# Optimization experiments

Hardware: AMD Instinct MI355X
Metric: run time of the kernel (lower is better)

## Reference

```python
import jax, jax.numpy as jnp
import numpy as np

H = 512   # hidden_size
E = 256   # embedding_size
V = 32000 # vocab_size
L = 1024  # max_length (encoder seq len)
B = 64    # batch


def setup_inputs() -> dict:
    key = jax.random.key(0)
    ks = jax.random.split(key, 18)
    n = lambda i, shape, s=0.05: (jax.random.normal(ks[i], shape, dtype=jnp.float32) * s)
    return {
        "input": jax.random.randint(ks[0], (B, 1), 0, V),
        "last_output_context": n(1, (1, B, H), 1.0),
        "last_hidden": n(2, (1, B, H), 1.0),
        "last_cell_state": n(3, (1, B, H), 1.0),
        "encoder_outputs": n(4, (L, B, H), 1.0),
        "emb": n(5, (V, E)),
        "W_ih": n(6, (4 * H, E + H)),
        "W_hh": n(7, (4 * H, H)),
        "b_ih": n(8, (4 * H,)),
        "b_hh": n(9, (4 * H,)),
        "W_attn": n(10, (H, 2 * H)),
        "b_attn": n(11, (H,)),
        "beta": n(12, (H, 1), 1.0),
        "W_oc": n(13, (H, 2 * H)),
        "b_oc": n(14, (H,)),
        "W_out": n(15, (V, H)),
        "b_out": n(16, (V,)),
    }


def reference(input, last_output_context, last_hidden, last_cell_state,
              encoder_outputs, emb, W_ih, W_hh, b_ih, b_hh,
              W_attn, b_attn, beta, W_oc, b_oc, W_out, b_out):
    # embedding lookup: (B,1) -> (B,E)  (permute(1,0,2) then squeeze step dim)
    tok = emb[input[:, 0]]                                   # (B, E)
    x = jnp.concatenate([tok, last_output_context[0]], axis=1)  # (B, E+H)
    # single-step LSTM (PyTorch gate order i, f, g, o)
    gates = x @ W_ih.T + last_hidden[0] @ W_hh.T + b_ih + b_hh  # (B, 4H)
    i_g, f_g, g_g, o_g = jnp.split(gates, 4, axis=1)
    i_g = jax.nn.sigmoid(i_g)
    f_g = jax.nn.sigmoid(f_g)
    g_g = jnp.tanh(g_g)
    o_g = jax.nn.sigmoid(o_g)
    c = f_g * last_cell_state[0] + i_g * g_g                  # (B, H)
    h = o_g * jnp.tanh(c)                                     # (B, H) == rnn_output
    # additive attention, vectorized over the seq_len loop
    h_tiled = jnp.broadcast_to(h[None], (L, B, H))
    cat = jnp.concatenate([h_tiled, encoder_outputs], axis=-1)  # (L, B, 2H)
    energy = jnp.tanh(cat @ W_attn.T + b_attn) @ beta           # (L, B, 1)
    attn_w = jax.nn.softmax(energy[..., 0], axis=0)             # (L, B) softmax over seq
    # context = bmm(attn_weights, encoder_outputs)
    context = jnp.einsum('lb,lbh->bh', attn_w, encoder_outputs)  # (B, H)
    co = jnp.tanh(jnp.concatenate([h, context], axis=1) @ W_oc.T + b_oc)  # (B, H)
    output = jax.nn.log_softmax(co @ W_out.T + b_out, axis=1)    # (B, V)
    return output, co[None], h[None], c[None]
```

## Files before the change

kernel.cpp:

```cpp
#include <hip/hip_runtime.h>
#include <hip/hip_bf16.h>
#include <cstddef>

#define H   512
#define E   256
#define V   32000
#define L   1024
#define B   64
#define KX  768
#define M_TOT 65536

typedef __attribute__((ext_vector_type(8))) _Float16 half8v;
typedef __attribute__((ext_vector_type(4))) float f32x4;

__global__ __launch_bounds__(256) void k_conv_w(const float* __restrict__ W_attn,
                                                unsigned short* __restrict__ Wf) {
    int e0 = blockIdx.x * 2048 + threadIdx.x * 8;
    int j = e0 >> 9, k = e0 & 511;
    const float* src = &W_attn[(size_t)j * (2 * H) + H + k];
    float4 x0 = *reinterpret_cast<const float4*>(src);
    float4 x1 = *reinterpret_cast<const float4*>(src + 4);
    float xs[8] = {x0.x, x0.y, x0.z, x0.w, x1.x, x1.y, x1.z, x1.w};
    union { half8v v; _Float16 u[8]; } hv;
    #pragma unroll
    for (int i = 0; i < 8; ++i) hv.u[i] = (_Float16)xs[i];
    *reinterpret_cast<half8v*>(&Wf[e0]) = hv.v;
}

__global__ __launch_bounds__(256) void k_build(const int* __restrict__ inp,
                                               const float* __restrict__ loc,
                                               const float* __restrict__ hprev,
                                               const float* __restrict__ emb,
                                               float* __restrict__ xprevT) {
    int gid = blockIdx.x * 256 + threadIdx.x;
    int k = gid >> 6, b = gid & 63;
    float v;
    if (k < 256)      v = emb[(size_t)inp[b] * E + k];
    else if (k < 768) v = loc[b * H + (k - 256)];
    else              v = hprev[b * H + (k - 768)];
    xprevT[gid] = v;
}

__global__ __launch_bounds__(256) void k_lstm(const float* __restrict__ W_ih,
                                              const float* __restrict__ W_hh,
                                              const float* __restrict__ b_ih,
                                              const float* __restrict__ b_hh,
                                              const float* __restrict__ xprevT,
                                              const float* __restrict__ cprev,
                                              float* __restrict__ h_out,
                                              float* __restrict__ c_out,
                                              float* __restrict__ hnewT) {
    int u = blockIdx.x;
    int w = threadIdx.x >> 6;
    int b = threadIdx.x & 63;
    int j = w * 512 + u;
    float a0 = 0.f, a1 = 0.f, a2 = 0.f, a3 = 0.f;
    const float* Wr = &W_ih[(size_t)j * KX];
    for (int k = 0; k < KX; k += 4) {
        float4 wv = *reinterpret_cast<const float4*>(&Wr[k]);
        a0 += wv.x * xprevT[(k + 0) * 64 + b];
        a1 += wv.y * xprevT[(k + 1) * 64 + b];
        a2 += wv.z * xprevT[(k + 2) * 64 + b];
        a3 += wv.w * xprevT[(k + 3) * 64 + b];
    }
    const float* Wr2 = &W_hh[(size_t)j * H];
    const float* hT = &xprevT[KX * 64];
    for (int k = 0; k < H; k += 4) {
        float4 wv = *reinterpret_cast<const float4*>(&Wr2[k]);
        a0 += wv.x * hT[(k + 0) * 64 + b];
        a1 += wv.y * hT[(k + 1) * 64 + b];
        a2 += wv.z * hT[(k + 2) * 64 + b];
        a3 += wv.w * hT[(k + 3) * 64 + b];
    }
    float acc = b_ih[j] + b_hh[j] + ((a0 + a1) + (a2 + a3));
    __shared__ float gs[4][64];
    gs[w][b] = acc;
    __syncthreads();
    if (threadIdx.x < 64) {
        float ig = 1.f / (1.f + __expf(-gs[0][b]));
        float fg = 1.f / (1.f + __expf(-gs[1][b]));
        float gg = tanhf(gs[2][b]);
        float og = 1.f / (1.f + __expf(-gs[3][b]));
        float c = fg * cprev[b * H + u] + ig * gg;
        float h = og * tanhf(c);
        c_out[b * H + u] = c;
        h_out[b * H + u] = h;
        hnewT[u * 64 + b] = h;
    }
}

__global__ __launch_bounds__(256) void k_hw(const float* __restrict__ W_attn,
                                            const float* __restrict__ b_attn,
                                            const float* __restrict__ hT,
                                            float* __restrict__ hW_jb) {
    int j = blockIdx.x * 4 + (threadIdx.x >> 6);
    int b = threadIdx.x & 63;
    float a0 = 0.f, a1 = 0.f, a2 = 0.f, a3 = 0.f;
    const float* Wr = &W_attn[(size_t)j * (2 * H)];
    for (int k = 0; k < H; k += 4) {
        float4 wv = *reinterpret_cast<const float4*>(&Wr[k]);
        a0 += wv.x * hT[(k + 0) * 64 + b];
        a1 += wv.y * hT[(k + 1) * 64 + b];
        a2 += wv.z * hT[(k + 2) * 64 + b];
        a3 += wv.w * hT[(k + 3) * 64 + b];
    }
    hW_jb[j * 64 + b] = b_attn[j] + ((a0 + a1) + (a2 + a3));
}

#define BKE 32
#define PITCH 40

__global__ __launch_bounds__(256, 4) void k_energy_v4(
        const float* __restrict__ enc,
        const unsigned short* __restrict__ Wf,
        const float* __restrict__ hW,
        const float* __restrict__ beta,
        float* __restrict__ partial_e) {
    __shared__ unsigned short Ah[128 * PITCH];
    __shared__ unsigned short Bh[128 * PITCH];
    __shared__ float red[2][128];

    const int tid  = threadIdx.x;
    const int lane = tid & 63;
    const int wave = tid >> 6;
    const int wm = wave >> 1;
    const int wn = wave & 1;
    const int mt = blockIdx.x >> 2;
    const int jt = blockIdx.x & 3;
    const int m0 = mt * 128;
    const int j0 = jt * 128;

    const int srow = tid >> 2;
    const int skc  = tid & 3;

    float4 ra0[2], ra1[2];
    half8v rb[2];
    #pragma unroll
    for (int p = 0; p < 2; ++p) {
        int row = p * 64 + srow;
        const float* asrc = &enc[(size_t)(m0 + row) * H + skc * 8];
        ra0[p] = *reinterpret_cast<const float4*>(asrc);
        ra1[p] = *reinterpret_cast<const float4*>(asrc + 4);
        rb[p] = *reinterpret_cast<const half8v*>(&Wf[(size_t)(j0 + row) * H + skc * 8]);
    }

    f32x4 acc[4][4];
    #pragma unroll
    for (int i = 0; i < 4; ++i)
        #pragma unroll
        for (int j = 0; j < 4; ++j) acc[i][j] = (f32x4){0.f, 0.f, 0.f, 0.f};

    for (int k0 = 0; k0 < H; k0 += BKE) {
        __syncthreads();
        #pragma unroll
        for (int p = 0; p < 2; ++p) {
            float xs[8] = {ra0[p].x, ra0[p].y, ra0[p].z, ra0[p].w,
                           ra1[p].x, ra1[p].y, ra1[p].z, ra1[p].w};
            union { half8v v; _Float16 u[8]; } hv;
            #pragma unroll
            for (int i = 0; i < 8; ++i) hv.u[i] = (_Float16)xs[i];
            int off = (p * 64 + srow) * PITCH + skc * 8;
            *reinterpret_cast<half8v*>(&Ah[off]) = hv.v;
            *reinterpret_cast<half8v*>(&Bh[off]) = rb[p];
        }
        __syncthreads();
        if (k0 + BKE < H) {
            int kn = k0 + BKE;
            #pragma unroll
            for (int p = 0; p < 2; ++p) {
                int row = p * 64 + srow;
                const float* asrc = &enc[(size_t)(m0 + row) * H + kn + skc * 8];
                ra0[p] = *reinterpret_cast<const float4*>(asrc);
                ra1[p] = *reinterpret_cast<const float4*>(asrc + 4);
                rb[p] = *reinterpret_cast<const half8v*>(&Wf[(size_t)(j0 + row) * H + kn + skc * 8]);
            }
        }
        const int fr = lane & 15;
        const int kb = (lane >> 4) * 8;
        half8v a_h[4], b_h[4];
        #pragma unroll
        for (int mf = 0; mf < 4; ++mf) {
            int off = (wm * 64 + mf * 16 + fr) * PITCH + kb;
            a_h[mf] = *reinterpret_cast<const half8v*>(&Ah[off]);
        }
        #pragma unroll
        for (int nf = 0; nf < 4; ++nf) {
            int off = (wn * 64 + nf * 16 + fr) * PITCH + kb;
            b_h[nf] = *reinterpret_cast<const half8v*>(&Bh[off]);
        }
        #pragma unroll
        for (int mf = 0; mf < 4; ++mf)
            #pragma unroll
            for (int nf = 0; nf < 4; ++nf)
                acc[mf][nf] = __builtin_amdgcn_mfma_f32_16x16x32_f16(
                    a_h[mf], b_h[nf], acc[mf][nf], 0, 0, 0);
    }
    float psum[4][4];
    #pragma unroll
    for (int i = 0; i < 4; ++i)
        #pragma unroll
        for (int r = 0; r < 4; ++r) psum[i][r] = 0.f;
    #pragma unroll
    for (int nf = 0; nf < 4; ++nf) {
        int jj = j0 + wn * 64 + nf * 16 + (lane & 15);
        float bet = beta[jj];
        #pragma unroll
        for (int mf = 0; mf < 4; ++mf) {
            int b_base = (wm * 64 + mf * 16 + (lane >> 4) * 4) & 63;
            float4 hw4 = *reinterpret_cast<const float4*>(&hW[jj * 64 + b_base]);
            float hwv[4] = {hw4.x, hw4.y, hw4.z, hw4.w};
            #pragma unroll
            for (int r = 0; r < 4; ++r) {
                float e = acc[mf][nf][r] + hwv[r];
                float ex = __expf(2.f * e);
                psum[mf][r] += bet * (1.f - 2.f / (ex + 1.f));
            }
        }
    }
    #pragma unroll
    for (int mf = 0; mf < 4; ++mf)
        #pragma unroll
        for (int r = 0; r < 4; ++r) {
            float v = psum[mf][r];
            v += __shfl_xor(v, 1);
            v += __shfl_xor(v, 2);
            v += __shfl_xor(v, 4);
            v += __shfl_xor(v, 8);
            psum[mf][r] = v;
        }
    __syncthreads();
    if ((lane & 15) == 0) {
        #pragma unroll
        for (int mf = 0; mf < 4; ++mf)
            #pragma unroll
            for (int r = 0; r < 4; ++r)
                red[wn][wm * 64 + mf * 16 + (lane >> 4) * 4 + r] = psum[mf][r];
    }
    __syncthreads();
    if (tid < 128)
        partial_e[(size_t)jt * M_TOT + m0 + tid] = red[0][tid] + red[1][tid];
}

__global__ __launch_bounds__(256) void k_softmax_l(const float* __restrict__ partial_e,
                                                   float* __restrict__ attn_w) {
    int b = blockIdx.x;
    int tid = threadIdx.x;
    float el[4];
    float m = -1e30f;
    #pragma unroll
    for (int i = 0; i < 4; ++i) {
        int l = i * 256 + tid;
        float e = 0.f;
        #pragma unroll
        for (int nb = 0; nb < 4; ++nb)
            e += partial_e[(size_t)nb * M_TOT + l * 64 + b];
        el[i] = e;
        m = fmaxf(m, e);
    }
    #pragma unroll
    for (int s = 1; s < 64; s <<= 1) m = fmaxf(m, __shfl_xor(m, s));
    __shared__ float redm[4];
    if ((tid & 63) == 0) redm[tid >> 6] = m;
    __syncthreads();
    m = fmaxf(fmaxf(redm[0], redm[1]), fmaxf(redm[2], redm[3]));
    float s = 0.f;
    #pragma unroll
    for (int i = 0; i < 4; ++i) { el[i] = __expf(el[i] - m); s += el[i]; }
    #pragma unroll
    for (int sh = 1; sh < 64; sh <<= 1) s += __shfl_xor(s, sh);
    __shared__ float reds[4];
    if ((tid & 63) == 0) reds[tid >> 6] = s;
    __syncthreads();
    s = reds[0] + reds[1] + reds[2] + reds[3];
    float inv = 1.f / s;
    #pragma unroll
    for (int i = 0; i < 4; ++i)
        attn_w[(i * 256 + tid) * 64 + b] = el[i] * inv;
}

__global__ __launch_bounds__(128) void k_ctx_part(const float* __restrict__ attn_w,
                                                  const float* __restrict__ enc,
                                                  float* __restrict__ ctx_part) {
    int chunk = blockIdx.x, b = blockIdx.y;
    int h = threadIdx.x * 4;
    float4 acc = {0.f, 0.f, 0.f, 0.f};
    for (int i = 0; i < 32; ++i) {
        int l = chunk * 32 + i;
        float w = attn_w[l * 64 + b];
        float4 e4 = *reinterpret_cast<const float4*>(
            &enc[((size_t)l * 64 + b) * H + h]);
        acc.x += w * e4.x;
        acc.y += w * e4.y;
        acc.z += w * e4.z;
        acc.w += w * e4.w;
    }
    *reinterpret_cast<float4*>(&ctx_part[((size_t)(chunk * 64 + b)) * H + h]) = acc;
}

__global__ __launch_bounds__(256) void k_ctx_reduce(const float* __restrict__ ctx_part,
                                                    float* __restrict__ ctxT) {
    int gid = blockIdx.x * 256 + threadIdx.x;
    int b = gid >> 9, h = gid & 511;
    float s = 0.f;
    for (int c = 0; c < 32; ++c)
        s += ctx_part[((size_t)(c * 64 + b)) * H + h];
    ctxT[h * 64 + b] = s;
}

__global__ __launch_bounds__(256) void k_co(const float* __restrict__ W_oc,
                                            const float* __restrict__ b_oc,
                                            const float* __restrict__ hT,
                                            const float* __restrict__ ctxT,
                                            float* __restrict__ co_out) {
    int j = blockIdx.x * 4 + (threadIdx.x >> 6);
    int b = threadIdx.x & 63;
    float a0 = 0.f, a1 = 0.f, a2 = 0.f, a3 = 0.f;
    const float* Wr = &W_oc[(size_t)j * (2 * H)];
    for (int k = 0; k < H; k += 4) {
        float4 wv = *reinterpret_cast<const float4*>(&Wr[k]);
        a0 += wv.x * hT[(k + 0) * 64 + b];
        a1 += wv.y * hT[(k + 1) * 64 + b];
        a2 += wv.z * hT[(k + 2) * 64 + b];
        a3 += wv.w * hT[(k + 3) * 64 + b];
    }
    const float* Wr2 = Wr + H;
    for (int k = 0; k < H; k += 4) {
        float4 wv = *reinterpret_cast<const float4*>(&Wr2[k]);
        a0 += wv.x * ctxT[(k + 0) * 64 + b];
        a1 += wv.y * ctxT[(k + 1) * 64 + b];
        a2 += wv.z * ctxT[(k + 2) * 64 + b];
        a3 += wv.w * ctxT[(k + 3) * 64 + b];
    }
    co_out[b * H + j] = tanhf(b_oc[j] + ((a0 + a1) + (a2 + a3)));
}

__global__ __launch_bounds__(256) void k_logits_v2(const float* __restrict__ co,
                                                   const float* __restrict__ W_out,
                                                   const float* __restrict__ b_out,
                                                   float* __restrict__ logits) {
    __shared__ unsigned short Ah[64 * PITCH];
    __shared__ unsigned short Bh[64 * PITCH];

    const int tid  = threadIdx.x;
    const int lane = tid & 63;
    const int wave = tid >> 6;
    const int wm = wave >> 1;
    const int wn = wave & 1;
    const int j0 = blockIdx.x * 64;

    const int srow = tid >> 2;
    const int skc  = tid & 3;

    float4 ra0, ra1, rb0, rb1;
    {
        const float* as = &co[(size_t)srow * H + skc * 8];
        ra0 = *reinterpret_cast<const float4*>(as);
        ra1 = *reinterpret_cast<const float4*>(as + 4);
        const float* bs = &W_out[(size_t)(j0 + srow) * H + skc * 8];
        rb0 = *reinterpret_cast<const float4*>(bs);
        rb1 = *reinterpret_cast<const float4*>(bs + 4);
    }

    f32x4 acc[2][2];
    #pragma unroll
    for (int i = 0; i < 2; ++i)
        #pragma unroll
        for (int j = 0; j < 2; ++j) acc[i][j] = (f32x4){0.f, 0.f, 0.f, 0.f};

    for (int k0 = 0; k0 < H; k0 += BKE) {
        __syncthreads();
        {
            float xs[8] = {ra0.x, ra0.y, ra0.z, ra0.w, ra1.x, ra1.y, ra1.z, ra1.w};
            union { half8v v; _Float16 u[8]; } ha;
            #pragma unroll
            for (int i = 0; i < 8; ++i) ha.u[i] = (_Float16)xs[i];
            float ys[8] = {rb0.x, rb0.y, rb0.z, rb0.w, rb1.x, rb1.y, rb1.z, rb1.w};
            union { half8v v; _Float16 u[8]; } hb;
            #pragma unroll
            for (int i = 0; i < 8; ++i) hb.u[i] = (_Float16)ys[i];
            int off = srow * PITCH + skc * 8;
            *reinterpret_cast<half8v*>(&Ah[off]) = ha.v;
            *reinterpret_cast<half8v*>(&Bh[off]) = hb.v;
        }
        __syncthreads();
        if (k0 + BKE < H) {
            int kn = k0 + BKE;
            const float* as = &co[(size_t)srow * H + kn + skc * 8];
            ra0 = *reinterpret_cast<const float4*>(as);
            ra1 = *reinterpret_cast<const float4*>(as + 4);
            const float* bs = &W_out[(size_t)(j0 + srow) * H + kn + skc * 8];
            rb0 = *reinterpret_cast<const float4*>(bs);
            rb1 = *reinterpret_cast<const float4*>(bs + 4);
        }
        const int fr = lane & 15;
        const int kb = (lane >> 4) * 8;
        half8v a_h[2], b_h[2];
        #pragma unroll
        for (int mf = 0; mf < 2; ++mf) {
            int off = (wm * 32 + mf * 16 + fr) * PITCH + kb;
            a_h[mf] = *reinterpret_cast<const half8v*>(&Ah[off]);
        }
        #pragma unroll
        for (int nf = 0; nf < 2; ++nf) {
            int off = (wn * 32 + nf * 16 + fr) * PITCH + kb;
            b_h[nf] = *reinterpret_cast<const half8v*>(&Bh[off]);
        }
        #pragma unroll
        for (int mf = 0; mf < 2; ++mf)
            #pragma unroll
            for (int nf = 0; nf < 2; ++nf)
                acc[mf][nf] = __builtin_amdgcn_mfma_f32_16x16x32_f16(
                    a_h[mf], b_h[nf], acc[mf][nf], 0, 0, 0);
    }
    #pragma unroll
    for (int nf = 0; nf < 2; ++nf) {
        int j = j0 + wn * 32 + nf * 16 + (lane & 15);
        float bo = b_out[j];
        #pragma unroll
        for (int mf = 0; mf < 2; ++mf) {
            int mbase = wm * 32 + mf * 16 + (lane >> 4) * 4;
            #pragma unroll
            for (int r = 0; r < 4; ++r)
                logits[(size_t)(mbase + r) * V + j] = acc[mf][nf][r] + bo;
        }
    }
}

__global__ __launch_bounds__(256) void k_lsm_part(const float* __restrict__ logits,
                                                  float* __restrict__ pmax,
                                                  float* __restrict__ psum) {
    int chunk = blockIdx.x, b = blockIdx.y;
    int tid = threadIdx.x;
    const float* row = &logits[(size_t)b * V + chunk * 4000];
    float v[16];
    float m = -1e30f;
    #pragma unroll
    for (int t = 0; t < 16; ++t) {
        int i = t * 256 + tid;
        v[t] = (i < 4000) ? row[i] : -1e30f;
        m = fmaxf(m, v[t]);
    }
    #pragma unroll
    for (int s = 1; s < 64; s <<= 1) m = fmaxf(m, __shfl_xor(m, s));
    __shared__ float redm[4];
    if ((tid & 63) == 0) redm[tid >> 6] = m;
    __syncthreads();
    m = fmaxf(fmaxf(redm[0], redm[1]), fmaxf(redm[2], redm[3]));
    float s = 0.f;
    #pragma unroll
    for (int t = 0; t < 16; ++t) s += __expf(v[t] - m);
    #pragma unroll
    for (int sh = 1; sh < 64; sh <<= 1) s += __shfl_xor(s, sh);
    __shared__ float reds[4];
    if ((tid & 63) == 0) reds[tid >> 6] = s;
    __syncthreads();
    if (tid == 0) {
        pmax[chunk * 64 + b] = m;
        psum[chunk * 64 + b] = reds[0] + reds[1] + reds[2] + reds[3];
    }
}

__global__ __launch_bounds__(64) void k_lsm_final(const float* __restrict__ pmax,
                                                  const float* __restrict__ psum,
                                                  float* __restrict__ lse) {
    int b = threadIdx.x;
    float m = -1e30f;
    #pragma unroll
    for (int c = 0; c < 8; ++c) m = fmaxf(m, pmax[c * 64 + b]);
    float s = 0.f;
    #pragma unroll
    for (int c = 0; c < 8; ++c) s += psum[c * 64 + b] * __expf(pmax[c * 64 + b] - m);
    lse[b] = m + __logf(s);
}

__global__ __launch_bounds__(256) void k_lsm_write(const float* __restrict__ logits,
                                                   const float* __restrict__ lse,
                                                   float* __restrict__ out) {
    size_t i4 = ((size_t)blockIdx.x * 256 + threadIdx.x) * 4;
    int b = (int)(i4 / V);
    float l = lse[b];
    float4 x = *reinterpret_cast<const float4*>(&logits[i4]);
    x.x -= l; x.y -= l; x.z -= l; x.w -= l;
    *reinterpret_cast<float4*>(&out[i4]) = x;
}

extern "C" void kernel_launch(void* const* d_in, const int* in_sizes, int n_in,
                              void* d_out, int out_size, void* d_ws, size_t ws_size,
                              hipStream_t stream) {
    const int*   inp    = (const int*)  d_in[0];
    const float* loc    = (const float*)d_in[1];
    const float* hprev  = (const float*)d_in[2];
    const float* cprev  = (const float*)d_in[3];
    const float* enc    = (const float*)d_in[4];
    const float* emb    = (const float*)d_in[5];
    const float* W_ih   = (const float*)d_in[6];
    const float* W_hh   = (const float*)d_in[7];
    const float* b_ih   = (const float*)d_in[8];
    const float* b_hh   = (const float*)d_in[9];
    const float* W_attn = (const float*)d_in[10];
    const float* b_attn = (const float*)d_in[11];
    const float* beta   = (const float*)d_in[12];
    const float* W_oc   = (const float*)d_in[13];
    const float* b_oc   = (const float*)d_in[14];
    const float* W_out  = (const float*)d_in[15];
    const float* b_out  = (const float*)d_in[16];

    float* out = (float*)d_out;
    float* out_co = out + (size_t)B * V;
    float* out_h  = out_co + B * H;
    float* out_c  = out_h  + B * H;

    float* ws = (float*)d_ws;
    float* xprevT = ws;
    float* hnewT  = xprevT + 1280 * 64;
    float* hW     = hnewT  + H * 64;
    float* pe     = hW     + H * 64;
    float* attnw  = pe     + 4 * M_TOT;
    float* ctxp   = attnw  + M_TOT;
    float* ctxT   = ctxp   + 32 * 64 * H;
    float* logits = ctxT   + H * 64;
    float* pmax   = logits + (size_t)B * V;
    float* psum   = pmax   + 512;
    float* lse    = psum   + 512;
    unsigned short* Wf = (unsigned short*)(lse + 64);

    k_conv_w<<<128, 256, 0, stream>>>(W_attn, Wf);
    k_build <<<320, 256, 0, stream>>>(inp, loc, hprev, emb, xprevT);
    k_lstm  <<<512, 256, 0, stream>>>(W_ih, W_hh, b_ih, b_hh, xprevT, cprev,
                                      out_h, out_c, hnewT);
    k_hw    <<<128, 256, 0, stream>>>(W_attn, b_attn, hnewT, hW);
    k_energy_v4<<<2048, 256, 0, stream>>>(enc, Wf, hW, beta, pe);
    k_softmax_l<<<64, 256, 0, stream>>>(pe, attnw);
    k_ctx_part <<<dim3(32, 64), 128, 0, stream>>>(attnw, enc, ctxp);
    k_ctx_reduce<<<128, 256, 0, stream>>>(ctxp, ctxT);
    k_co    <<<128, 256, 0, stream>>>(W_oc, b_oc, hnewT, ctxT, out_co);
    k_logits_v2<<<500, 256, 0, stream>>>(out_co, W_out, b_out, logits);
    k_lsm_part<<<dim3(8, 64), 256, 0, stream>>>(logits, pmax, psum);
    k_lsm_final<<<1, 64, 0, stream>>>(pmax, psum, lse);
    k_lsm_write<<<2000, 256, 0, stream>>>(logits, lse, out);
}
```

Baseline: 257.1 us.

## Deepen energy GEMM K-tile, remap blocks per XCD, raise MFMA priority

The attention-energy GEMM kernel now uses a K step of 64 instead of 32, which halves the number of barrier/stage iterations and issues 32 MFMAs per stage. It also remaps block indices so the four j-tiles of one M tile, which read the same encoder rows, are consecutive in the per-XCD (bid&7) ordering, to improve L2 reuse of the encoder rows. s_setprio is raised around the MFMA burst. In exchange, more registers are needed for the prefetch buffers and LDS use roughly doubles, which may reduce occupancy under launch_bounds(256,4). The logits kernel keeps its old tile constants under new names.

```diff
diff --git a/kernel.cpp b/kernel.cpp
--- a/kernel.cpp
+++ b/kernel.cpp
@@ -107,17 +107,17 @@
     hW_jb[j * 64 + b] = b_attn[j] + ((a0 + a1) + (a2 + a3));
 }
 
-#define BKE 32
-#define PITCH 40
-
-__global__ __launch_bounds__(256, 4) void k_energy_v4(
+#define BKE 64
+#define PITCHE 72
+
+__global__ __launch_bounds__(256, 4) void k_energy_v5(
         const float* __restrict__ enc,
         const unsigned short* __restrict__ Wf,
         const float* __restrict__ hW,
         const float* __restrict__ beta,
         float* __restrict__ partial_e) {
-    __shared__ unsigned short Ah[128 * PITCH];
-    __shared__ unsigned short Bh[128 * PITCH];
+    __shared__ unsigned short Ah[128 * PITCHE];
+    __shared__ unsigned short Bh[128 * PITCHE];
     __shared__ float red[2][128];
 
     const int tid  = threadIdx.x;
@@ -125,23 +125,26 @@
     const int wave = tid >> 6;
     const int wm = wave >> 1;
     const int wn = wave & 1;
-    const int mt = blockIdx.x >> 2;
-    const int jt = blockIdx.x & 3;
+    const int bid = blockIdx.x;
+    const int xcd = bid & 7;
+    const int loc = bid >> 3;
+    const int mt  = xcd * 64 + (loc >> 2);
+    const int jt  = loc & 3;
     const int m0 = mt * 128;
     const int j0 = jt * 128;
 
-    const int srow = tid >> 2;
-    const int skc  = tid & 3;
-
-    float4 ra0[2], ra1[2];
-    half8v rb[2];
-    #pragma unroll
-    for (int p = 0; p < 2; ++p) {
-        int row = p * 64 + srow;
-        const float* asrc = &enc[(size_t)(m0 + row) * H + skc * 8];
+    const int q  = tid & 7;
+    const int r0 = tid >> 3;
+
+    float4 ra0[4], ra1[4];
+    half8v rb[4];
+    #pragma unroll
+    for (int p = 0; p < 4; ++p) {
+        int row = p * 32 + r0;
+        const float* asrc = &enc[(size_t)(m0 + row) * H + q * 8];
         ra0[p] = *reinterpret_cast<const float4*>(asrc);
         ra1[p] = *reinterpret_cast<const float4*>(asrc + 4);
-        rb[p] = *reinterpret_cast<const half8v*>(&Wf[(size_t)(j0 + row) * H + skc * 8]);
+        rb[p] = *reinterpret_cast<const half8v*>(&Wf[(size_t)(j0 + row) * H + q * 8]);
     }
 
     f32x4 acc[4][4];
@@ -153,13 +156,13 @@
     for (int k0 = 0; k0 < H; k0 += BKE) {
         __syncthreads();
         #pragma unroll
-        for (int p = 0; p < 2; ++p) {
+        for (int p = 0; p < 4; ++p) {
             float xs[8] = {ra0[p].x, ra0[p].y, ra0[p].z, ra0[p].w,
                            ra1[p].x, ra1[p].y, ra1[p].z, ra1[p].w};
             union { half8v v; _Float16 u[8]; } hv;
             #pragma unroll
             for (int i = 0; i < 8; ++i) hv.u[i] = (_Float16)xs[i];
-            int off = (p * 64 + srow) * PITCH + skc * 8;
+            int off = (p * 32 + r0) * PITCHE + q * 8;
             *reinterpret_cast<half8v*>(&Ah[off]) = hv.v;
             *reinterpret_cast<half8v*>(&Bh[off]) = rb[p];
         }
@@ -167,33 +170,39 @@
         if (k0 + BKE < H) {
             int kn = k0 + BKE;
             #pragma unroll
-            for (int p = 0; p < 2; ++p) {
-                int row = p * 64 + srow;
-                const float* asrc = &enc[(size_t)(m0 + row) * H + kn + skc * 8];
+            for (int p = 0; p < 4; ++p) {
+                int row = p * 32 + r0;
+                const float* asrc = &enc[(size_t)(m0 + row) * H + kn + q * 8];
                 ra0[p] = *reinterpret_cast<const float4*>(asrc);
                 ra1[p] = *reinterpret_cast<const float4*>(asrc + 4);
-                rb[p] = *reinterpret_cast<const half8v*>(&Wf[(size_t)(j0 + row) * H + kn + skc * 8]);
+                rb[p] = *reinterpret_cast<const half8v*>(&Wf[(size_t)(j0 + row) * H + kn + q * 8]);
             }
         }
         const int fr = lane & 15;
         const int kb = (lane >> 4) * 8;
-        half8v a_h[4], b_h[4];
+        half8v a_h[4][2], b_h[4][2];
         #pragma unroll
         for (int mf = 0; mf < 4; ++mf) {
-            int off = (wm * 64 + mf * 16 + fr) * PITCH + kb;
-            a_h[mf] = *reinterpret_cast<const half8v*>(&Ah[off]);
+            int off = (wm * 64 + mf * 16 + fr) * PITCHE + kb;
+            a_h[mf][0] = *reinterpret_cast<const half8v*>(&Ah[off]);
+            a_h[mf][1] = *reinterpret_cast<const half8v*>(&Ah[off + 32]);
         }
         #pragma unroll
         for (int nf = 0; nf < 4; ++nf) {
-            int off = (wn * 64 + nf * 16 + fr) * PITCH + kb;
-            b_h[nf] = *reinterpret_cast<const half8v*>(&Bh[off]);
-        }
-        #pragma unroll
-        for (int mf = 0; mf < 4; ++mf)
-            #pragma unroll
-            for (int nf = 0; nf < 4; ++nf)
-                acc[mf][nf] = __builtin_amdgcn_mfma_f32_16x16x32_f16(
-                    a_h[mf], b_h[nf], acc[mf][nf], 0, 0, 0);
+            int off = (wn * 64 + nf * 16 + fr) * PITCHE + kb;
+            b_h[nf][0] = *reinterpret_cast<const half8v*>(&Bh[off]);
+            b_h[nf][1] = *reinterpret_cast<const half8v*>(&Bh[off + 32]);
+        }
+        __builtin_amdgcn_s_setprio(1);
+        #pragma unroll
+        for (int ks = 0; ks < 2; ++ks)
+            #pragma unroll
+            for (int mf = 0; mf < 4; ++mf)
+                #pragma unroll
+                for (int nf = 0; nf < 4; ++nf)
+                    acc[mf][nf] = __builtin_amdgcn_mfma_f32_16x16x32_f16(
+                        a_h[mf][ks], b_h[nf][ks], acc[mf][nf], 0, 0, 0);
+        __builtin_amdgcn_s_setprio(0);
     }
     float psum[4][4];
     #pragma unroll
@@ -334,12 +343,14 @@
     co_out[b * H + j] = tanhf(b_oc[j] + ((a0 + a1) + (a2 + a3)));
 }
 
+#define BKL 32
+#define PITCHL 40
 __global__ __launch_bounds__(256) void k_logits_v2(const float* __restrict__ co,
                                                    const float* __restrict__ W_out,
                                                    const float* __restrict__ b_out,
                                                    float* __restrict__ logits) {
-    __shared__ unsigned short Ah[64 * PITCH];
-    __shared__ unsigned short Bh[64 * PITCH];
+    __shared__ unsigned short Ah[64 * PITCHL];
+    __shared__ unsigned short Bh[64 * PITCHL];
 
     const int tid  = threadIdx.x;
     const int lane = tid & 63;
@@ -367,7 +378,7 @@
         #pragma unroll
         for (int j = 0; j < 2; ++j) acc[i][j] = (f32x4){0.f, 0.f, 0.f, 0.f};
 
-    for (int k0 = 0; k0 < H; k0 += BKE) {
+    for (int k0 = 0; k0 < H; k0 += BKL) {
         __syncthreads();
         {
             float xs[8] = {ra0.x, ra0.y, ra0.z, ra0.w, ra1.x, ra1.y, ra1.z, ra1.w};
@@ -378,13 +389,13 @@
             union { half8v v; _Float16 u[8]; } hb;
             #pragma unroll
             for (int i = 0; i < 8; ++i) hb.u[i] = (_Float16)ys[i];
-            int off = srow * PITCH + skc * 8;
+            int off = srow * PITCHL + skc * 8;
             *reinterpret_cast<half8v*>(&Ah[off]) = ha.v;
             *reinterpret_cast<half8v*>(&Bh[off]) = hb.v;
         }
         __syncthreads();
-        if (k0 + BKE < H) {
-            int kn = k0 + BKE;
+        if (k0 + BKL < H) {
+            int kn = k0 + BKL;
             const float* as = &co[(size_t)srow * H + kn + skc * 8];
             ra0 = *reinterpret_cast<const float4*>(as);
             ra1 = *reinterpret_cast<const float4*>(as + 4);
@@ -397,12 +408,12 @@
         half8v a_h[2], b_h[2];
         #pragma unroll
         for (int mf = 0; mf < 2; ++mf) {
-            int off = (wm * 32 + mf * 16 + fr) * PITCH + kb;
+            int off = (wm * 32 + mf * 16 + fr) * PITCHL + kb;
             a_h[mf] = *reinterpret_cast<const half8v*>(&Ah[off]);
         }
         #pragma unroll
         for (int nf = 0; nf < 2; ++nf) {
-            int off = (wn * 32 + nf * 16 + fr) * PITCH + kb;
+            int off = (wn * 32 + nf * 16 + fr) * PITCHL + kb;
             b_h[nf] = *reinterpret_cast<const half8v*>(&Bh[off]);
         }
         #pragma unroll
@@ -529,7 +540,7 @@
     k_lstm  <<<512, 256, 0, stream>>>(W_ih, W_hh, b_ih, b_hh, xprevT, cprev,
                                       out_h, out_c, hnewT);
     k_hw    <<<128, 256, 0, stream>>>(W_attn, b_attn, hnewT, hW);
-    k_energy_v4<<<2048, 256, 0, stream>>>(enc, Wf, hW, beta, pe);
+    k_energy_v5<<<2048, 256, 0, stream>>>(enc, Wf, hW, beta, pe);
     k_softmax_l<<<64, 256, 0, stream>>>(pe, attnw);
     k_ctx_part <<<dim3(32, 64), 128, 0, stream>>>(attnw, enc, ctxp);
     k_ctx_reduce<<<128, 256, 0, stream>>>(ctxp, ctxT);
```

Measured after the change: 591.6 us. +130.1%, slower.

## Restructure energy GEMM to full-K tiles and drop LDS staging in logits

Applied to the files above, without the earlier changes.

The energy kernel now loads each 64-row block of encoder outputs into shared memory once, converted to fp16 over the full K range. Each wave reads its 128 attention-weight columns straight from global memory, so one block covers all 512 output columns. This removes the 4-way split over j, the partial-energy buffer and the per-k-tile barriers, and the softmax reads a single energy value per position. The logits kernel drops shared-memory staging and converts W_out and co fragments directly in registers. The risks are lower occupancy from about 65KB of LDS and the larger accumulator array, plus uncoalesced global fragment loads for the B operands.

```diff
diff --git a/kernel.cpp b/kernel.cpp
--- a/kernel.cpp
+++ b/kernel.cpp
@@ -13,6 +13,15 @@
 typedef __attribute__((ext_vector_type(8))) _Float16 half8v;
 typedef __attribute__((ext_vector_type(4))) float f32x4;
 
+__device__ __forceinline__ half8v cvt8(float4 x0, float4 x1) {
+    union { half8v v; _Float16 u[8]; } hv;
+    hv.u[0] = (_Float16)x0.x; hv.u[1] = (_Float16)x0.y;
+    hv.u[2] = (_Float16)x0.z; hv.u[3] = (_Float16)x0.w;
+    hv.u[4] = (_Float16)x1.x; hv.u[5] = (_Float16)x1.y;
+    hv.u[6] = (_Float16)x1.z; hv.u[7] = (_Float16)x1.w;
+    return hv.v;
+}
+
 __global__ __launch_bounds__(256) void k_conv_w(const float* __restrict__ W_attn,
                                                 unsigned short* __restrict__ Wf) {
     int e0 = blockIdx.x * 2048 + threadIdx.x * 8;
@@ -20,11 +29,8 @@
     const float* src = &W_attn[(size_t)j * (2 * H) + H + k];
     float4 x0 = *reinterpret_cast<const float4*>(src);
     float4 x1 = *reinterpret_cast<const float4*>(src + 4);
-    float xs[8] = {x0.x, x0.y, x0.z, x0.w, x1.x, x1.y, x1.z, x1.w};
-    union { half8v v; _Float16 u[8]; } hv;
-    #pragma unroll
-    for (int i = 0; i < 8; ++i) hv.u[i] = (_Float16)xs[i];
-    *reinterpret_cast<half8v*>(&Wf[e0]) = hv.v;
+    half8v hv = cvt8(x0, x1);
+    *reinterpret_cast<half8v*>(&Wf[e0]) = hv;
 }
 
 __global__ __launch_bounds__(256) void k_build(const int* __restrict__ inp,
@@ -107,106 +113,75 @@
     hW_jb[j * 64 + b] = b_attn[j] + ((a0 + a1) + (a2 + a3));
 }
 
-#define BKE 32
-#define PITCH 40
-
-__global__ __launch_bounds__(256, 4) void k_energy_v4(
+#define EPITCH 520
+
+__global__ __launch_bounds__(256, 2) void k_energy_v6(
         const float* __restrict__ enc,
         const unsigned short* __restrict__ Wf,
         const float* __restrict__ hW,
         const float* __restrict__ beta,
-        float* __restrict__ partial_e) {
-    __shared__ unsigned short Ah[128 * PITCH];
-    __shared__ unsigned short Bh[128 * PITCH];
-    __shared__ float red[2][128];
+        float* __restrict__ energy) {
+    __shared__ unsigned short As[64 * EPITCH];
+    __shared__ float red[4][64];
 
     const int tid  = threadIdx.x;
     const int lane = tid & 63;
-    const int wave = tid >> 6;
-    const int wm = wave >> 1;
-    const int wn = wave & 1;
-    const int mt = blockIdx.x >> 2;
-    const int jt = blockIdx.x & 3;
-    const int m0 = mt * 128;
-    const int j0 = jt * 128;
-
-    const int srow = tid >> 2;
-    const int skc  = tid & 3;
-
-    float4 ra0[2], ra1[2];
-    half8v rb[2];
-    #pragma unroll
-    for (int p = 0; p < 2; ++p) {
-        int row = p * 64 + srow;
-        const float* asrc = &enc[(size_t)(m0 + row) * H + skc * 8];
-        ra0[p] = *reinterpret_cast<const float4*>(asrc);
-        ra1[p] = *reinterpret_cast<const float4*>(asrc + 4);
-        rb[p] = *reinterpret_cast<const half8v*>(&Wf[(size_t)(j0 + row) * H + skc * 8]);
-    }
-
-    f32x4 acc[4][4];
+    const int w    = tid >> 6;
+    const int m0   = blockIdx.x * 64;
+
+    {
+        int row = tid >> 2;
+        int kbase = (tid & 3) * 128;
+        const float* src = &enc[(size_t)(m0 + row) * H + kbase];
+        #pragma unroll
+        for (int c = 0; c < 16; ++c) {
+            float4 x0 = *reinterpret_cast<const float4*>(src + c * 8);
+            float4 x1 = *reinterpret_cast<const float4*>(src + c * 8 + 4);
+            half8v hv = cvt8(x0, x1);
+            *reinterpret_cast<half8v*>(&As[row * EPITCH + kbase + c * 8]) = hv;
+        }
+    }
+    __syncthreads();
+
+    const int fr = lane & 15;
+    const int kb = (lane >> 4) * 8;
+
+    f32x4 acc[4][8];
+    #pragma unroll
+    for (int mf = 0; mf < 4; ++mf)
+        #pragma unroll
+        for (int nf = 0; nf < 8; ++nf) acc[mf][nf] = (f32x4){0.f, 0.f, 0.f, 0.f};
+
+    const unsigned short* Bbase = &Wf[(size_t)(w * 128 + fr) * H + kb];
+
+    for (int k0 = 0; k0 < H; k0 += 32) {
+        half8v a_h[4];
+        #pragma unroll
+        for (int mf = 0; mf < 4; ++mf)
+            a_h[mf] = *reinterpret_cast<const half8v*>(
+                &As[(mf * 16 + fr) * EPITCH + k0 + kb]);
+        #pragma unroll
+        for (int nf = 0; nf < 8; ++nf) {
+            half8v b_h = *reinterpret_cast<const half8v*>(&Bbase[(size_t)nf * 16 * H + k0]);
+            #pragma unroll
+            for (int mf = 0; mf < 4; ++mf)
+                acc[mf][nf] = __builtin_amdgcn_mfma_f32_16x16x32_f16(
+                    a_h[mf], b_h, acc[mf][nf], 0, 0, 0);
+        }
+    }
+
+    float psum[4][4];
     #pragma unroll
     for (int i = 0; i < 4; ++i)
         #pragma unroll
-        for (int j = 0; j < 4; ++j) acc[i][j] = (f32x4){0.f, 0.f, 0.f, 0.f};
-
-    for (int k0 = 0; k0 < H; k0 += BKE) {
-        __syncthreads();
-        #pragma unroll
-        for (int p = 0; p < 2; ++p) {
-            float xs[8] = {ra0[p].x, ra0[p].y, ra0[p].z, ra0[p].w,
-                           ra1[p].x, ra1[p].y, ra1[p].z, ra1[p].w};
-            union { half8v v; _Float16 u[8]; } hv;
-            #pragma unroll
-            for (int i = 0; i < 8; ++i) hv.u[i] = (_Float16)xs[i];
-            int off = (p * 64 + srow) * PITCH + skc * 8;
-            *reinterpret_cast<half8v*>(&Ah[off]) = hv.v;
-            *reinterpret_cast<half8v*>(&Bh[off]) = rb[p];
-        }
-        __syncthreads();
-        if (k0 + BKE < H) {
-            int kn = k0 + BKE;
-            #pragma unroll
-            for (int p = 0; p < 2; ++p) {
-                int row = p * 64 + srow;
-                const float* asrc = &enc[(size_t)(m0 + row) * H + kn + skc * 8];
-                ra0[p] = *reinterpret_cast<const float4*>(asrc);
-                ra1[p] = *reinterpret_cast<const float4*>(asrc + 4);
-                rb[p] = *reinterpret_cast<const half8v*>(&Wf[(size_t)(j0 + row) * H + kn + skc * 8]);
-            }
-        }
-        const int fr = lane & 15;
-        const int kb = (lane >> 4) * 8;
-        half8v a_h[4], b_h[4];
+        for (int r = 0; r < 4; ++r) psum[i][r] = 0.f;
+    #pragma unroll
+    for (int nf = 0; nf < 8; ++nf) {
+        int jj = w * 128 + nf * 16 + fr;
+        float bet = beta[jj];
         #pragma unroll
         for (int mf = 0; mf < 4; ++mf) {
-            int off = (wm * 64 + mf * 16 + fr) * PITCH + kb;
-            a_h[mf] = *reinterpret_cast<const half8v*>(&Ah[off]);
-        }
-        #pragma unroll
-        for (int nf = 0; nf < 4; ++nf) {
-            int off = (wn * 64 + nf * 16 + fr) * PITCH + kb;
-            b_h[nf] = *reinterpret_cast<const half8v*>(&Bh[off]);
-        }
-        #pragma unroll
-        for (int mf = 0; mf < 4; ++mf)
-            #pragma unroll
-            for (int nf = 0; nf < 4; ++nf)
-                acc[mf][nf] = __builtin_amdgcn_mfma_f32_16x16x32_f16(
-                    a_h[mf], b_h[nf], acc[mf][nf], 0, 0, 0);
-    }
-    float psum[4][4];
-    #pragma unroll
-    for (int i = 0; i < 4; ++i)
-        #pragma unroll
-        for (int r = 0; r < 4; ++r) psum[i][r] = 0.f;
-    #pragma unroll
-    for (int nf = 0; nf < 4; ++nf) {
-        int jj = j0 + wn * 64 + nf * 16 + (lane & 15);
-        float bet = beta[jj];
-        #pragma unroll
-        for (int mf = 0; mf < 4; ++mf) {
-            int b_base = (wm * 64 + mf * 16 + (lane >> 4) * 4) & 63;
+            int b_base = mf * 16 + (lane >> 4) * 4;
             float4 hw4 = *reinterpret_cast<const float4*>(&hW[jj * 64 + b_base]);
             float hwv[4] = {hw4.x, hw4.y, hw4.z, hw4.w};
             #pragma unroll
@@ -228,20 +203,19 @@
             v += __shfl_xor(v, 8);
             psum[mf][r] = v;
         }
-    __syncthreads();
-    if ((lane & 15) == 0) {
+    if (fr == 0) {
         #pragma unroll
         for (int mf = 0; mf < 4; ++mf)
             #pragma unroll
             for (int r = 0; r < 4; ++r)
-                red[wn][wm * 64 + mf * 16 + (lane >> 4) * 4 + r] = psum[mf][r];
-    }
-    __syncthreads();
-    if (tid < 128)
-        partial_e[(size_t)jt * M_TOT + m0 + tid] = red[0][tid] + red[1][tid];
-}
-
-__global__ __launch_bounds__(256) void k_softmax_l(const float* __restrict__ partial_e,
+                red[w][mf * 16 + (lane >> 4) * 4 + r] = psum[mf][r];
+    }
+    __syncthreads();
+    if (tid < 64)
+        energy[m0 + tid] = (red[0][tid] + red[1][tid]) + (red[2][tid] + red[3][tid]);
+}
+
+__global__ __launch_bounds__(256) void k_softmax_l(const float* __restrict__ energy,
                                                    float* __restrict__ attn_w) {
     int b = blockIdx.x;
     int tid = threadIdx.x;
@@ -250,10 +224,7 @@
     #pragma unroll
     for (int i = 0; i < 4; ++i) {
         int l = i * 256 + tid;
-        float e = 0.f;
-        #pragma unroll
-        for (int nb = 0; nb < 4; ++nb)
-            e += partial_e[(size_t)nb * M_TOT + l * 64 + b];
+        float e = energy[l * 64 + b];
         el[i] = e;
         m = fmaxf(m, e);
     }
@@ -334,95 +305,44 @@
     co_out[b * H + j] = tanhf(b_oc[j] + ((a0 + a1) + (a2 + a3)));
 }
 
-__global__ __launch_bounds__(256) void k_logits_v2(const float* __restrict__ co,
+__global__ __launch_bounds__(256) void k_logits_v3(const float* __restrict__ co,
                                                    const float* __restrict__ W_out,
                                                    const float* __restrict__ b_out,
                                                    float* __restrict__ logits) {
-    __shared__ unsigned short Ah[64 * PITCH];
-    __shared__ unsigned short Bh[64 * PITCH];
-
     const int tid  = threadIdx.x;
     const int lane = tid & 63;
-    const int wave = tid >> 6;
-    const int wm = wave >> 1;
-    const int wn = wave & 1;
-    const int j0 = blockIdx.x * 64;
-
-    const int srow = tid >> 2;
-    const int skc  = tid & 3;
-
-    float4 ra0, ra1, rb0, rb1;
-    {
-        const float* as = &co[(size_t)srow * H + skc * 8];
-        ra0 = *reinterpret_cast<const float4*>(as);
-        ra1 = *reinterpret_cast<const float4*>(as + 4);
-        const float* bs = &W_out[(size_t)(j0 + srow) * H + skc * 8];
-        rb0 = *reinterpret_cast<const float4*>(bs);
-        rb1 = *reinterpret_cast<const float4*>(bs + 4);
-    }
-
-    f32x4 acc[2][2];
-    #pragma unroll
-    for (int i = 0; i < 2; ++i)
-        #pragma unroll
-        for (int j = 0; j < 2; ++j) acc[i][j] = (f32x4){0.f, 0.f, 0.f, 0.f};
-
-    for (int k0 = 0; k0 < H; k0 += BKE) {
-        __syncthreads();
-        {
-            float xs[8] = {ra0.x, ra0.y, ra0.z, ra0.w, ra1.x, ra1.y, ra1.z, ra1.w};
-            union { half8v v; _Float16 u[8]; } ha;
-            #pragma unroll
-            for (int i = 0; i < 8; ++i) ha.u[i] = (_Float16)xs[i];
-            float ys[8] = {rb0.x, rb0.y, rb0.z, rb0.w, rb1.x, rb1.y, rb1.z, rb1.w};
-            union { half8v v; _Float16 u[8]; } hb;
-            #pragma unroll
-            for (int i = 0; i < 8; ++i) hb.u[i] = (_Float16)ys[i];
-            int off = srow * PITCH + skc * 8;
-            *reinterpret_cast<half8v*>(&Ah[off]) = ha.v;
-            *reinterpret_cast<half8v*>(&Bh[off]) = hb.v;
+    const int w    = tid >> 6;
+    const int fr   = lane & 15;
+    const int kb   = (lane >> 4) * 8;
+    const int j    = blockIdx.x * 64 + w * 16 + fr;
+
+    f32x4 acc[4];
+    #pragma unroll
+    for (int mf = 0; mf < 4; ++mf) acc[mf] = (f32x4){0.f, 0.f, 0.f, 0.f};
+
+    const float* Arow = &co[(size_t)fr * H + kb];
+    const float* Brow = &W_out[(size_t)j * H + kb];
+
+    for (int k0 = 0; k0 < H; k0 += 32) {
+        float4 b0 = *reinterpret_cast<const float4*>(Brow + k0);
+        float4 b1 = *reinterpret_cast<const float4*>(Brow + k0 + 4);
+        half8v bh = cvt8(b0, b1);
+        #pragma unroll
+        for (int mf = 0; mf < 4; ++mf) {
+            const float* ap = Arow + (size_t)mf * 16 * H + k0;
+            float4 a0 = *reinterpret_cast<const float4*>(ap);
+            float4 a1 = *reinterpret_cast<const float4*>(ap + 4);
+            half8v ah = cvt8(a0, a1);
+            acc[mf] = __builtin_amdgcn_mfma_f32_16x16x32_f16(ah, bh, acc[mf], 0, 0, 0);
         }
-        __syncthreads();
-        if (k0 + BKE < H) {
-            int kn = k0 + BKE;
-            const float* as = &co[(size_t)srow * H + kn + skc * 8];
-            ra0 = *reinterpret_cast<const float4*>(as);
-            ra1 = *reinterpret_cast<const float4*>(as + 4);
-            const float* bs = &W_out[(size_t)(j0 + srow) * H + kn + skc * 8];
-            rb0 = *reinterpret_cast<const float4*>(bs);
-            rb1 = *reinterpret_cast<const float4*>(bs + 4);
-        }
-        const int fr = lane & 15;
-        const int kb = (lane >> 4) * 8;
-        half8v a_h[2], b_h[2];
-        #pragma unroll
-        for (int mf = 0; mf < 2; ++mf) {
-            int off = (wm * 32 + mf * 16 + fr) * PITCH + kb;
-            a_h[mf] = *reinterpret_cast<const half8v*>(&Ah[off]);
-        }
-        #pragma unroll
-        for (int nf = 0; nf < 2; ++nf) {
-            int off = (wn * 32 + nf * 16 + fr) * PITCH + kb;
-            b_h[nf] = *reinterpret_cast<const half8v*>(&Bh[off]);
-        }
-        #pragma unroll
-        for (int mf = 0; mf < 2; ++mf)
-            #pragma unroll
-            for (int nf = 0; nf < 2; ++nf)
-                acc[mf][nf] = __builtin_amdgcn_mfma_f32_16x16x32_f16(
-                    a_h[mf], b_h[nf], acc[mf][nf], 0, 0, 0);
-    }
-    #pragma unroll
-    for (int nf = 0; nf < 2; ++nf) {
-        int j = j0 + wn * 32 + nf * 16 + (lane & 15);
-        float bo = b_out[j];
-        #pragma unroll
-        for (int mf = 0; mf < 2; ++mf) {
-            int mbase = wm * 32 + mf * 16 + (lane >> 4) * 4;
-            #pragma unroll
-            for (int r = 0; r < 4; ++r)
-                logits[(size_t)(mbase + r) * V + j] = acc[mf][nf][r] + bo;
-        }
+    }
+    float bo = b_out[j];
+    #pragma unroll
+    for (int mf = 0; mf < 4; ++mf) {
+        int mbase = mf * 16 + (lane >> 4) * 4;
+        #pragma unroll
+        for (int r = 0; r < 4; ++r)
+            logits[(size_t)(mbase + r) * V + j] = acc[mf][r] + bo;
     }
 }
 
@@ -514,8 +434,8 @@
     float* xprevT = ws;
     float* hnewT  = xprevT + 1280 * 64;
     float* hW     = hnewT  + H * 64;
-    float* pe     = hW     + H * 64;
-    float* attnw  = pe     + 4 * M_TOT;
+    float* energy = hW     + H * 64;
+    float* attnw  = energy + M_TOT;
     float* ctxp   = attnw  + M_TOT;
     float* ctxT   = ctxp   + 32 * 64 * H;
     float* logits = ctxT   + H * 64;
@@ -529,12 +449,12 @@
     k_lstm  <<<512, 256, 0, stream>>>(W_ih, W_hh, b_ih, b_hh, xprevT, cprev,
                                       out_h, out_c, hnewT);
     k_hw    <<<128, 256, 0, stream>>>(W_attn, b_attn, hnewT, hW);
-    k_energy_v4<<<2048, 256, 0, stream>>>(enc, Wf, hW, beta, pe);
-    k_softmax_l<<<64, 256, 0, stream>>>(pe, attnw);
+    k_energy_v6<<<1024, 256, 0, stream>>>(enc, Wf, hW, beta, energy);
+    k_softmax_l<<<64, 256, 0, stream>>>(energy, attnw);
     k_ctx_part <<<dim3(32, 64), 128, 0, stream>>>(attnw, enc, ctxp);
     k_ctx_reduce<<<128, 256, 0, stream>>>(ctxp, ctxT);
     k_co    <<<128, 256, 0, stream>>>(W_oc, b_oc, hnewT, ctxT, out_co);
-    k_logits_v2<<<500, 256, 0, stream>>>(out_co, W_out, b_out, logits);
+    k_logits_v3<<<500, 256, 0, stream>>>(out_co, W_out, b_out, logits);
     k_lsm_part<<<dim3(8, 64), 256, 0, stream>>>(logits, pmax, psum);
     k_lsm_final<<<1, 64, 0, stream>>>(pmax, psum, lse);
     k_lsm_write<<<2000, 256, 0, stream>>>(logits, lse, out);
```

After: 313.2 us. +21.8%, slower.
